# Optimization experiments

Measured on AMD Instinct MI355X. Metric: run time of the kernel, lower is better.

## Reference

```python
import jax, jax.numpy as jnp
import numpy as np

MAX_SEQ_LEN = 4096
N_QUBITS = 11
N_LAYERS = 2
DIM = 2 ** N_QUBITS


def setup_inputs() -> dict:
    key = jax.random.key(0)
    k_theta, = jax.random.split(key, 1)
    # matches nn.Parameter(torch.randn(max_seq_len, n_layers, 3*n_qubits) * 0.1)
    theta = jax.random.normal(k_theta, (MAX_SEQ_LEN, N_LAYERS, 3 * N_QUBITS), dtype=jnp.float32) * 0.1
    positions = jnp.arange(MAX_SEQ_LEN, dtype=jnp.int32)
    return {"theta": theta, "positions": positions}


def _gate_matrices(theta_sel):
    """theta_sel: (B, L, 3Q) -> combined single-qubit unitaries U = Rz @ Ry @ Rx, (B, L, Q, 2, 2) complex64."""
    B = theta_sel.shape[0]
    ang = theta_sel.reshape(B, N_LAYERS, N_QUBITS, 3) * 0.5  # half angles
    a, b, g = ang[..., 0], ang[..., 1], ang[..., 2]  # rx, ry, rz
    ca, sa = jnp.cos(a), jnp.sin(a)
    cb, sb = jnp.cos(b), jnp.sin(b)
    zero = jnp.zeros_like(a) + 0j
    # RX(t) = [[cos t/2, -i sin t/2], [-i sin t/2, cos t/2]]
    Rx = jnp.stack([jnp.stack([ca + 0j, -1j * sa], -1),
                    jnp.stack([-1j * sa, ca + 0j], -1)], -2)
    # RY(t) = [[cos, -sin], [sin, cos]]
    Ry = jnp.stack([jnp.stack([cb + 0j, -sb + 0j], -1),
                    jnp.stack([sb + 0j, cb + 0j], -1)], -2)
    # RZ(t) = diag(e^{-it/2}, e^{+it/2})
    Rz = jnp.stack([jnp.stack([jnp.exp(-1j * g), zero], -1),
                    jnp.stack([zero, jnp.exp(1j * g)], -1)], -2)
    return jnp.einsum('...ij,...jk,...kl->...il', Rz, Ry, Rx).astype(jnp.complex64)


def _simulate(theta_sel):
    """Batched little-endian statevector simulation of the PQC. Returns (B, 2^Q) float32 (real part)."""
    B = theta_sel.shape[0]
    U = _gate_matrices(theta_sel)  # (B, L, Q, 2, 2)
    state = jnp.zeros((B, DIM), jnp.complex64).at[:, 0].set(1.0)  # |0...0>
    for l in range(N_LAYERS):
        # single-qubit RX.RY.RZ block (fused per qubit)
        for q in range(N_QUBITS):
            # qubit q has stride 2^q in little-endian index
            st = state.reshape(B, 2 ** (N_QUBITS - 1 - q), 2, 2 ** q)
            state = jnp.einsum('bij,bhjl->bhil', U[:, l, q], st).reshape(B, DIM)
        # CX ladder: cx(q, q+1) -> control bit q, target bit q+1
        for q in range(N_QUBITS - 1):
            st = state.reshape(B, 2 ** (N_QUBITS - 2 - q), 2, 2, 2 ** q)  # (B, rest, target, control, low)
            c0 = st[:, :, :, 0, :]
            c1 = st[:, :, ::-1, 1, :]  # flip target when control = 1
            state = jnp.stack([c0, c1], axis=3).reshape(B, DIM)
    return state.real.astype(jnp.float32)


def reference(theta, positions):
    return _simulate(theta[positions])
```

## Files before the change

kernel.cpp:

```cpp
#include <hip/hip_runtime.h>
#include <math.h>

#define N_QUBITS 11
#define N_LAYERS 2
#define DIM 2048
#define N_GATES 22
#define ROW 36

typedef float v2f __attribute__((ext_vector_type(2)));
static __device__ __forceinline__ v2f splat(float s) { return (v2f){s, s}; }


static __device__ __forceinline__ int nofm(int m) {
    int n = 0, p = 0;
    #pragma unroll
    for (int q = 0; q < 5; ++q) { p ^= (m >> q) & 1; n |= p << q; }
    return n;
}

static __device__ __forceinline__ float getS(const v2f (&S)[16], int n) {
    return (n & 1) ? S[n >> 1].y : S[n >> 1].x;
}
static __device__ __forceinline__ void setS(v2f (&S)[16], int n, float v) {
    if (n & 1) S[n >> 1].y = v; else S[n >> 1].x = v;
}

static __device__ __forceinline__
void apply5(v2f (&SR)[16], v2f (&SI)[16], const float (*G)[8], int gbase)
{
    {
        const float4 gA = *(const float4*)&G[gbase][0];
        const float4 gB = *(const float4*)&G[gbase][4];
        const v2f C0r = {gA.x, gB.x}, C0i = {gA.y, gB.y};
        const v2f C1r = {gA.z, gB.z}, C1i = {gA.w, gB.w};
        #pragma unroll
        for (int k = 0; k < 16; ++k) {
            const v2f rx = splat(SR[k].x), ry = splat(SR[k].y);
            const v2f ix = splat(SI[k].x), iy = splat(SI[k].y);
            SR[k] = C0r * rx - C0i * ix + C1r * ry - C1i * iy;
            SI[k] = C0r * ix + C0i * rx + C1r * iy + C1i * ry;
        }
    }
    #pragma unroll
    for (int t = 1; t < 5; ++t) {
        const float4 gA = *(const float4*)&G[gbase + t][0];
        const float4 gB = *(const float4*)&G[gbase + t][4];
        const v2f u00r = splat(gA.x), u00i = splat(gA.y);
        const v2f u01r = splat(gA.z), u01i = splat(gA.w);
        const v2f u10r = splat(gB.x), u10i = splat(gB.y);
        const v2f u11r = splat(gB.z), u11i = splat(gB.w);
        const int h = 1 << (t - 1);
        #pragma unroll
        for (int s = 0; s < 8; ++s) {
            const int k0 = ((s >> (t - 1)) << t) | (s & (h - 1));
            const int k1 = k0 + h;
            const v2f ar = SR[k0], ai = SI[k0];
            const v2f br = SR[k1], bi = SI[k1];
            SR[k0] = u00r * ar - u00i * ai + u01r * br - u01i * bi;
            SI[k0] = u00r * ai + u00i * ar + u01r * bi + u01i * br;
            SR[k1] = u10r * ar - u10i * ai + u11r * br - u11i * bi;
            SI[k1] = u10r * ai + u10i * ar + u11r * bi + u11i * br;
        }
    }
}

static __device__ __forceinline__
void lane_gate_q10(v2f (&SR)[16], v2f (&SI)[16], const float* g, int L)
{
    const int bit = (L >> 5) & 1;
    const v2f csr = splat(bit ? g[6] : g[0]), csi = splat(bit ? g[7] : g[1]);
    const v2f cpr = splat(bit ? g[4] : g[2]), cpi = splat(bit ? g[5] : g[3]);
    #pragma unroll
    for (int k = 0; k < 16; ++k) {
        const double dr = __builtin_bit_cast(double, SR[k]);
        const double di = __builtin_bit_cast(double, SI[k]);
        const v2f pr = __builtin_bit_cast(v2f, __shfl_xor(dr, 32));
        const v2f pi = __builtin_bit_cast(v2f, __shfl_xor(di, 32));
        const v2f ar = SR[k], ai = SI[k];
        SR[k] = csr * ar - csi * ai + cpr * pr - cpi * pi;
        SI[k] = csr * ai + csi * ar + cpr * pi + cpi * pr;
    }
}

static __device__ __forceinline__
void write_rows(float* buf, const v2f (&S)[16], int L)
{
    #pragma unroll
    for (int k = 0; k < 8; ++k) {
        *(float4*)&buf[L * ROW + 4 * k] =
            make_float4(S[2*k].x, S[2*k].y, S[2*k+1].x, S[2*k+1].y);
    }
}

static __device__ __forceinline__
void read_swap(const float* buf, v2f (&S)[16], int L)
{
    const int rb = L & 32;
    const int rr = L & 31;
    #pragma unroll
    for (int t = 0; t < 16; ++t) {
        const float a0 = buf[(2*t     | rb) * ROW + rr];
        const float a1 = buf[((2*t+1) | rb) * ROW + rr];
        S[t] = (v2f){a0, a1};
    }
}

static __device__ __forceinline__
void read_cnot(const float* buf, v2f (&S)[16], int L)
{
    const int gl      = (L ^ (L << 1)) & 31;
    const int lane_or = ((((L >> 5) ^ (L >> 4)) & 1) << 5);
    #pragma unroll
    for (int t = 0; t < 16; ++t) {
        const int n0 = 2 * t, n1 = 2 * t + 1;
        const int f0 = (n0 ^ (n0 << 1)) & 31;
        const int f1 = (n1 ^ (n1 << 1)) & 31;
        const int reg = gl ^ (n0 >> 4);
        const float a0 = buf[(f0 | lane_or) * ROW + reg];
        const float a1 = buf[(f1 | lane_or) * ROW + reg];
        S[t] = (v2f){a0, a1};
    }
}

__global__ __launch_bounds__(64) __attribute__((amdgpu_waves_per_eu(4, 4)))
void pqc_sim_kernel(const float* __restrict__ theta,
                    const int* __restrict__ positions,
                    float* __restrict__ out)
{
    __shared__ float G[N_GATES][8];
    __shared__ float buf[64 * ROW];

    const int b   = blockIdx.x;
    const int L   = threadIdx.x;
    const int pos = positions[b];

    if (L < N_GATES) {
        const int l = L / N_QUBITS;
        const int q = L % N_QUBITS;
        const float* th = theta + (((size_t)pos * N_LAYERS + l) * (3 * N_QUBITS)) + 3 * q;
        const float a  = th[0] * 0.5f;
        const float bb = th[1] * 0.5f;
        const float g  = th[2] * 0.5f;
        float sa, ca, sb, cb, sg, cg;
        sincosf(a,  &sa, &ca);
        sincosf(bb, &sb, &cb);
        sincosf(g,  &sg, &cg);
        const float m00r =  cb * ca, m00i =  sb * sa;
        const float m01r = -sb * ca, m01i = -cb * sa;
        const float m10r =  sb * ca, m10i = -cb * sa;
        const float m11r =  cb * ca, m11i = -sb * sa;
        G[L][0] = m00r * cg + m00i * sg;  G[L][1] = m00i * cg - m00r * sg;
        G[L][2] = m01r * cg + m01i * sg;  G[L][3] = m01i * cg - m01r * sg;
        G[L][4] = m10r * cg - m10i * sg;  G[L][5] = m10i * cg + m10r * sg;
        G[L][6] = m11r * cg - m11i * sg;  G[L][7] = m11i * cg + m11r * sg;
    }
    __syncthreads();

    v2f SR[16], SI[16];

    {
        float car0[5], cai0[5], car1[5], cai1[5];
        #pragma unroll
        for (int q = 0; q < 5; ++q) {
            car0[q] = G[q][0]; cai0[q] = G[q][1];
            car1[q] = G[q][4]; cai1[q] = G[q][5];
        }
        setS(SR, nofm(0), car0[0]);  setS(SI, nofm(0), cai0[0]);
        setS(SR, nofm(1), car1[0]);  setS(SI, nofm(1), cai1[0]);
        #pragma unroll
        for (int q = 1; q < 5; ++q) {
            #pragma unroll
            for (int m = 0; m < (1 << q); ++m) {
                const int ns = nofm(m);
                const int nd = nofm(m | (1 << q));
                const float ar = getS(SR, ns), ai = getS(SI, ns);
                setS(SR, nd, ar * car1[q] - ai * cai1[q]);
                setS(SI, nd, ar * cai1[q] + ai * car1[q]);
                setS(SR, ns, ar * car0[q] - ai * cai0[q]);
                setS(SI, ns, ar * cai0[q] + ai * car0[q]);
            }
        }

        const int x = L ^ (L >> 1);
        float plr, pli;
        {
            const int bq = x & 1;
            plr = bq ? G[6][4] : G[6][0];
            pli = bq ? G[6][5] : G[6][1];
        }
        #pragma unroll
        for (int k = 1; k < 5; ++k) {
            const int bq = (x >> k) & 1;
            const float cr = bq ? G[6 + k][4] : G[6 + k][0];
            const float ci = bq ? G[6 + k][5] : G[6 + k][1];
            const float tr = plr * cr - pli * ci;
            pli = plr * ci + pli * cr;
            plr = tr;
        }
        const int l0 = L & 1;
        const float c5ar = l0 ? G[5][4] : G[5][0];
        const float c5ai = l0 ? G[5][5] : G[5][1];
        const float c5br = l0 ? G[5][0] : G[5][4];
        const float c5bi = l0 ? G[5][1] : G[5][5];
        const float F0r = plr * c5ar - pli * c5ai, F0i = plr * c5ai + pli * c5ar;
        const float F1r = plr * c5br - pli * c5bi, F1i = plr * c5bi + pli * c5br;

        #pragma unroll
        for (int n = 0; n < 32; ++n) {
            const float fr = (n & 16) ? F1r : F0r;
            const float fi = (n & 16) ? F1i : F0i;
            const float ar = getS(SR, n), ai = getS(SI, n);
            setS(SR, n, ar * fr - ai * fi);
            setS(SI, n, ar * fi + ai * fr);
        }
    }

    apply5(SR, SI, G, 11);
    write_rows(buf, SR, L);  read_swap(buf, SR, L);
    write_rows(buf, SI, L);  read_swap(buf, SI, L);
    apply5(SR, SI, G, 16);
    lane_gate_q10(SR, SI, G[21], L);
    write_rows(buf, SR, L);  read_cnot(buf, SR, L);

    float* orow = out + (size_t)b * DIM + L * 32;
    #pragma unroll
    for (int k = 0; k < 8; ++k) {
        *(float4*)(orow + 4 * k) =
            make_float4(SR[2*k].x, SR[2*k].y, SR[2*k+1].x, SR[2*k+1].y);
    }
}

extern "C" void kernel_launch(void* const* d_in, const int* in_sizes, int n_in,
                              void* d_out, int out_size, void* d_ws, size_t ws_size,
                              hipStream_t stream)
{
    const float* theta     = (const float*)d_in[0];
    const int*   positions = (const int*)d_in[1];
    float*       out       = (float*)d_out;
    const int B = in_sizes[1];

    pqc_sim_kernel<<<B, 64, 0, stream>>>(theta, positions, out);
}
```

Before: 89.95 us.

## Split statevector across two waves with cross-wave LDS exchange for final gate

Each block now uses two wavefronts of 64 lanes, each holding 16 amplitudes per lane instead of 32, which halves register pressure and doubles the threads per sample. Qubits 8 and 9 are applied with lane shuffles, and the qubit-10 gate of the last layer, fused with the CNOT permutation, is done by exchanging halves through shared memory with extra barriers. Only the real part is computed at the end, and first-layer gate storage is trimmed to the columns that act on |0>. The cost is extra __syncthreads and LDS traffic across waves, and the occupancy attribute is removed.

```diff
diff --git a/kernel.cpp b/kernel.cpp
--- a/kernel.cpp
+++ b/kernel.cpp
@@ -2,31 +2,27 @@
 #include <math.h>
 
 #define N_QUBITS 11
-#define N_LAYERS 2
 #define DIM 2048
-#define N_GATES 22
-#define ROW 36
 
 typedef float v2f __attribute__((ext_vector_type(2)));
 static __device__ __forceinline__ v2f splat(float s) { return (v2f){s, s}; }
 
 
-static __device__ __forceinline__ int nofm(int m) {
+static __device__ __forceinline__ float getS(const v2f (&S)[8], int n) {
+    return (n & 1) ? S[n >> 1].y : S[n >> 1].x;
+}
+static __device__ __forceinline__ void setS(v2f (&S)[8], int n, float v) {
+    if (n & 1) S[n >> 1].y = v; else S[n >> 1].x = v;
+}
+static __device__ __forceinline__ int nofm4(int m) {
     int n = 0, p = 0;
     #pragma unroll
-    for (int q = 0; q < 5; ++q) { p ^= (m >> q) & 1; n |= p << q; }
+    for (int q = 0; q < 4; ++q) { p ^= (m >> q) & 1; n |= p << q; }
     return n;
 }
 
-static __device__ __forceinline__ float getS(const v2f (&S)[16], int n) {
-    return (n & 1) ? S[n >> 1].y : S[n >> 1].x;
-}
-static __device__ __forceinline__ void setS(v2f (&S)[16], int n, float v) {
-    if (n & 1) S[n >> 1].y = v; else S[n >> 1].x = v;
-}
-
 static __device__ __forceinline__
-void apply5(v2f (&SR)[16], v2f (&SI)[16], const float (*G)[8], int gbase)
+void apply4(v2f (&SR)[8], v2f (&SI)[8], const float (*G)[8], int gbase)
 {
     {
         const float4 gA = *(const float4*)&G[gbase][0];
@@ -34,7 +30,7 @@
         const v2f C0r = {gA.x, gB.x}, C0i = {gA.y, gB.y};
         const v2f C1r = {gA.z, gB.z}, C1i = {gA.w, gB.w};
         #pragma unroll
-        for (int k = 0; k < 16; ++k) {
+        for (int k = 0; k < 8; ++k) {
             const v2f rx = splat(SR[k].x), ry = splat(SR[k].y);
             const v2f ix = splat(SI[k].x), iy = splat(SI[k].y);
             SR[k] = C0r * rx - C0i * ix + C1r * ry - C1i * iy;
@@ -42,7 +38,7 @@
         }
     }
     #pragma unroll
-    for (int t = 1; t < 5; ++t) {
+    for (int t = 1; t < 4; ++t) {
         const float4 gA = *(const float4*)&G[gbase + t][0];
         const float4 gB = *(const float4*)&G[gbase + t][4];
         const v2f u00r = splat(gA.x), u00i = splat(gA.y);
@@ -51,7 +47,7 @@
         const v2f u11r = splat(gB.z), u11i = splat(gB.w);
         const int h = 1 << (t - 1);
         #pragma unroll
-        for (int s = 0; s < 8; ++s) {
+        for (int s = 0; s < 4; ++s) {
             const int k0 = ((s >> (t - 1)) << t) | (s & (h - 1));
             const int k1 = k0 + h;
             const v2f ar = SR[k0], ai = SI[k0];
@@ -65,79 +61,41 @@
 }
 
 static __device__ __forceinline__
-void lane_gate_q10(v2f (&SR)[16], v2f (&SI)[16], const float* g, int L)
-{
-    const int bit = (L >> 5) & 1;
+void shfl_gate(v2f (&SR)[8], v2f (&SI)[8], const float* g, int bit, int mask)
+{
     const v2f csr = splat(bit ? g[6] : g[0]), csi = splat(bit ? g[7] : g[1]);
     const v2f cpr = splat(bit ? g[4] : g[2]), cpi = splat(bit ? g[5] : g[3]);
     #pragma unroll
-    for (int k = 0; k < 16; ++k) {
+    for (int k = 0; k < 8; ++k) {
         const double dr = __builtin_bit_cast(double, SR[k]);
         const double di = __builtin_bit_cast(double, SI[k]);
-        const v2f pr = __builtin_bit_cast(v2f, __shfl_xor(dr, 32));
-        const v2f pi = __builtin_bit_cast(v2f, __shfl_xor(di, 32));
+        const v2f pr = __builtin_bit_cast(v2f, __shfl_xor(dr, mask));
+        const v2f pi = __builtin_bit_cast(v2f, __shfl_xor(di, mask));
         const v2f ar = SR[k], ai = SI[k];
         SR[k] = csr * ar - csi * ai + cpr * pr - cpi * pi;
         SI[k] = csr * ai + csi * ar + cpr * pi + cpi * pr;
     }
 }
 
-static __device__ __forceinline__
-void write_rows(float* buf, const v2f (&S)[16], int L)
-{
-    #pragma unroll
-    for (int k = 0; k < 8; ++k) {
-        *(float4*)&buf[L * ROW + 4 * k] =
-            make_float4(S[2*k].x, S[2*k].y, S[2*k+1].x, S[2*k+1].y);
-    }
-}
-
-static __device__ __forceinline__
-void read_swap(const float* buf, v2f (&S)[16], int L)
-{
-    const int rb = L & 32;
-    const int rr = L & 31;
-    #pragma unroll
-    for (int t = 0; t < 16; ++t) {
-        const float a0 = buf[(2*t     | rb) * ROW + rr];
-        const float a1 = buf[((2*t+1) | rb) * ROW + rr];
-        S[t] = (v2f){a0, a1};
-    }
-}
-
-static __device__ __forceinline__
-void read_cnot(const float* buf, v2f (&S)[16], int L)
-{
-    const int gl      = (L ^ (L << 1)) & 31;
-    const int lane_or = ((((L >> 5) ^ (L >> 4)) & 1) << 5);
-    #pragma unroll
-    for (int t = 0; t < 16; ++t) {
-        const int n0 = 2 * t, n1 = 2 * t + 1;
-        const int f0 = (n0 ^ (n0 << 1)) & 31;
-        const int f1 = (n1 ^ (n1 << 1)) & 31;
-        const int reg = gl ^ (n0 >> 4);
-        const float a0 = buf[(f0 | lane_or) * ROW + reg];
-        const float a1 = buf[(f1 | lane_or) * ROW + reg];
-        S[t] = (v2f){a0, a1};
-    }
-}
-
-__global__ __launch_bounds__(64) __attribute__((amdgpu_waves_per_eu(4, 4)))
+__global__ __launch_bounds__(128)
 void pqc_sim_kernel(const float* __restrict__ theta,
                     const int* __restrict__ positions,
                     float* __restrict__ out)
 {
-    __shared__ float G[N_GATES][8];
-    __shared__ float buf[64 * ROW];
-
-    const int b   = blockIdx.x;
-    const int L   = threadIdx.x;
+    __shared__ float G2[N_QUBITS][8];
+    __shared__ float C1[N_QUBITS][4];
+    __shared__ float buf[2176];
+
+    const int t = threadIdx.x;
+    const int w = t >> 6;
+    const int L = t & 63;
+    const int b = blockIdx.x;
     const int pos = positions[b];
 
-    if (L < N_GATES) {
-        const int l = L / N_QUBITS;
-        const int q = L % N_QUBITS;
-        const float* th = theta + (((size_t)pos * N_LAYERS + l) * (3 * N_QUBITS)) + 3 * q;
+    if (t < 22) {
+        const int l = t / N_QUBITS;
+        const int q = t % N_QUBITS;
+        const float* th = theta + (((size_t)pos * 2 + l) * (3 * N_QUBITS)) + 3 * q;
         const float a  = th[0] * 0.5f;
         const float bb = th[1] * 0.5f;
         const float g  = th[2] * 0.5f;
@@ -149,84 +107,131 @@
         const float m01r = -sb * ca, m01i = -cb * sa;
         const float m10r =  sb * ca, m10i = -cb * sa;
         const float m11r =  cb * ca, m11i = -sb * sa;
-        G[L][0] = m00r * cg + m00i * sg;  G[L][1] = m00i * cg - m00r * sg;
-        G[L][2] = m01r * cg + m01i * sg;  G[L][3] = m01i * cg - m01r * sg;
-        G[L][4] = m10r * cg - m10i * sg;  G[L][5] = m10i * cg + m10r * sg;
-        G[L][6] = m11r * cg - m11i * sg;  G[L][7] = m11i * cg + m11r * sg;
-    }
-    __syncthreads();
-
-    v2f SR[16], SI[16];
+        const float u00r = m00r * cg + m00i * sg, u00i = m00i * cg - m00r * sg;
+        const float u01r = m01r * cg + m01i * sg, u01i = m01i * cg - m01r * sg;
+        const float u10r = m10r * cg - m10i * sg, u10i = m10i * cg + m10r * sg;
+        const float u11r = m11r * cg - m11i * sg, u11i = m11i * cg + m11r * sg;
+        if (l) {
+            G2[q][0] = u00r; G2[q][1] = u00i; G2[q][2] = u01r; G2[q][3] = u01i;
+            G2[q][4] = u10r; G2[q][5] = u10i; G2[q][6] = u11r; G2[q][7] = u11i;
+        } else {
+            C1[q][0] = u00r; C1[q][1] = u00i;
+            C1[q][2] = u10r; C1[q][3] = u10i;
+        }
+    }
+    __syncthreads();
+
+    v2f SR[8], SI[8];
 
     {
-        float car0[5], cai0[5], car1[5], cai1[5];
-        #pragma unroll
-        for (int q = 0; q < 5; ++q) {
-            car0[q] = G[q][0]; cai0[q] = G[q][1];
-            car1[q] = G[q][4]; cai1[q] = G[q][5];
-        }
-        setS(SR, nofm(0), car0[0]);  setS(SI, nofm(0), cai0[0]);
-        setS(SR, nofm(1), car1[0]);  setS(SI, nofm(1), cai1[0]);
-        #pragma unroll
-        for (int q = 1; q < 5; ++q) {
+        setS(SR, 0,  C1[0][0]);  setS(SI, 0,  C1[0][1]);
+        setS(SR, 15, C1[0][2]);  setS(SI, 15, C1[0][3]);
+        #pragma unroll
+        for (int q = 1; q < 4; ++q) {
+            const float c0r = C1[q][0], c0i = C1[q][1];
+            const float c1r = C1[q][2], c1i = C1[q][3];
             #pragma unroll
             for (int m = 0; m < (1 << q); ++m) {
-                const int ns = nofm(m);
-                const int nd = nofm(m | (1 << q));
+                const int ns = nofm4(m), nd = nofm4(m | (1 << q));
                 const float ar = getS(SR, ns), ai = getS(SI, ns);
-                setS(SR, nd, ar * car1[q] - ai * cai1[q]);
-                setS(SI, nd, ar * cai1[q] + ai * car1[q]);
-                setS(SR, ns, ar * car0[q] - ai * cai0[q]);
-                setS(SI, ns, ar * cai0[q] + ai * car0[q]);
+                setS(SR, nd, ar * c1r - ai * c1i);
+                setS(SI, nd, ar * c1i + ai * c1r);
+                setS(SR, ns, ar * c0r - ai * c0i);
+                setS(SI, ns, ar * c0i + ai * c0r);
             }
         }
-
-        const int x = L ^ (L >> 1);
+        const int z = (L ^ (L << 1)) >> 1;
         float plr, pli;
+        { const int o = (z & 1) ? 2 : 0; plr = C1[5][o]; pli = C1[5][o + 1]; }
+        #pragma unroll
+        for (int k = 1; k < 5; ++k) {
+            const int o = ((z >> k) & 1) ? 2 : 0;
+            const float cr = C1[5 + k][o], ci = C1[5 + k][o + 1];
+            const float tr = plr * cr - pli * ci;
+            pli = plr * ci + pli * cr;  plr = tr;
+        }
         {
-            const int bq = x & 1;
-            plr = bq ? G[6][4] : G[6][0];
-            pli = bq ? G[6][5] : G[6][1];
-        }
-        #pragma unroll
-        for (int k = 1; k < 5; ++k) {
-            const int bq = (x >> k) & 1;
-            const float cr = bq ? G[6 + k][4] : G[6 + k][0];
-            const float ci = bq ? G[6 + k][5] : G[6 + k][1];
+            const int o = (w ^ ((L >> 5) & 1)) ? 2 : 0;
+            const float cr = C1[10][o], ci = C1[10][o + 1];
             const float tr = plr * cr - pli * ci;
-            pli = plr * ci + pli * cr;
-            plr = tr;
+            pli = plr * ci + pli * cr;  plr = tr;
         }
         const int l0 = L & 1;
-        const float c5ar = l0 ? G[5][4] : G[5][0];
-        const float c5ai = l0 ? G[5][5] : G[5][1];
-        const float c5br = l0 ? G[5][0] : G[5][4];
-        const float c5bi = l0 ? G[5][1] : G[5][5];
-        const float F0r = plr * c5ar - pli * c5ai, F0i = plr * c5ai + pli * c5ar;
-        const float F1r = plr * c5br - pli * c5bi, F1i = plr * c5bi + pli * c5br;
-
-        #pragma unroll
-        for (int n = 0; n < 32; ++n) {
-            const float fr = (n & 16) ? F1r : F0r;
-            const float fi = (n & 16) ? F1i : F0i;
-            const float ar = getS(SR, n), ai = getS(SI, n);
-            setS(SR, n, ar * fr - ai * fi);
-            setS(SI, n, ar * fi + ai * fr);
-        }
-    }
-
-    apply5(SR, SI, G, 11);
-    write_rows(buf, SR, L);  read_swap(buf, SR, L);
-    write_rows(buf, SI, L);  read_swap(buf, SI, L);
-    apply5(SR, SI, G, 16);
-    lane_gate_q10(SR, SI, G[21], L);
-    write_rows(buf, SR, L);  read_cnot(buf, SR, L);
-
-    float* orow = out + (size_t)b * DIM + L * 32;
-    #pragma unroll
-    for (int k = 0; k < 8; ++k) {
+        const float e0r = C1[4][l0 ? 2 : 0], e0i = C1[4][l0 ? 3 : 1];
+        const float e1r = C1[4][l0 ? 0 : 2], e1i = C1[4][l0 ? 1 : 3];
+        const float F0r = plr * e0r - pli * e0i, F0i = plr * e0i + pli * e0r;
+        const float F1r = plr * e1r - pli * e1i, F1i = plr * e1i + pli * e1r;
+        #pragma unroll
+        for (int k = 0; k < 8; ++k) {
+            const v2f fr = splat(k < 4 ? F0r : F1r);
+            const v2f fi = splat(k < 4 ? F0i : F1i);
+            const v2f r = SR[k], i = SI[k];
+            SR[k] = r * fr - i * fi;
+            SI[k] = r * fi + i * fr;
+        }
+    }
+
+    apply4(SR, SI, G2, 0);
+
+    {
+        float* reg = buf + w * 1088;
+        const int hi = L & 48;
+        const int cs = L & 15;
+        #pragma unroll
+        for (int n = 0; n < 16; ++n) reg[L * 17 + n] = getS(SR, n);
+        #pragma unroll
+        for (int n = 0; n < 16; ++n) setS(SR, n, reg[(n + hi) * 17 + cs]);
+        #pragma unroll
+        for (int n = 0; n < 16; ++n) reg[L * 17 + n] = getS(SI, n);
+        #pragma unroll
+        for (int n = 0; n < 16; ++n) setS(SI, n, reg[(n + hi) * 17 + cs]);
+    }
+
+    apply4(SR, SI, G2, 4);
+    shfl_gate(SR, SI, G2[8], (L >> 4) & 1, 16);
+    shfl_gate(SR, SI, G2[9], (L >> 5) & 1, 32);
+
+    const int f10 = w ^ ((L >> 5) & 1);
+    const float u0r = G2[10][f10 * 4 + 0], u0i = G2[10][f10 * 4 + 1];
+    const float u1r = G2[10][f10 * 4 + 2], u1i = G2[10][f10 * 4 + 3];
+    const int ls_hi = (L ^ (L << 1)) & 48;
+    const int nsx   = (L ^ (L << 1)) & 15;
+    float outv[16];
+
+    __syncthreads();
+    if (w == 0) {
+        #pragma unroll
+        for (int n = 0; n < 16; ++n) {
+            buf[L * 17 + n]        = getS(SR, n);
+            buf[1088 + L * 17 + n] = getS(SI, n);
+        }
+    }
+    __syncthreads();
+    #pragma unroll
+    for (int n = 0; n < 16; ++n) {
+        const int a = (((n ^ (n << 1)) & 15) | ls_hi) * 17 + (nsx ^ (n >> 3));
+        outv[n] = u0r * buf[a] - u0i * buf[1088 + a];
+    }
+    __syncthreads();
+    if (w == 1) {
+        #pragma unroll
+        for (int n = 0; n < 16; ++n) {
+            buf[L * 17 + n]        = getS(SR, n);
+            buf[1088 + L * 17 + n] = getS(SI, n);
+        }
+    }
+    __syncthreads();
+    #pragma unroll
+    for (int n = 0; n < 16; ++n) {
+        const int a = (((n ^ (n << 1)) & 15) | ls_hi) * 17 + (nsx ^ (n >> 3));
+        outv[n] += u1r * buf[a] - u1i * buf[1088 + a];
+    }
+
+    float* orow = out + (size_t)b * DIM + w * 1024 + L * 16;
+    #pragma unroll
+    for (int k = 0; k < 4; ++k) {
         *(float4*)(orow + 4 * k) =
-            make_float4(SR[2*k].x, SR[2*k].y, SR[2*k+1].x, SR[2*k+1].y);
+            make_float4(outv[4*k], outv[4*k+1], outv[4*k+2], outv[4*k+3]);
     }
 }
 
@@ -239,5 +244,5 @@
     float*       out       = (float*)d_out;
     const int B = in_sizes[1];
 
-    pqc_sim_kernel<<<B, 64, 0, stream>>>(theta, positions, out);
-}
+    pqc_sim_kernel<<<B, 128, 0, stream>>>(theta, positions, out);
+}
```

Result: faster. 86.39 us (-4.0%).
